# Performance work log

Measured on AMD Instinct MI355X. Metric: run time of the kernel, lower is better.

## Reference

```python
import jax, jax.numpy as jnp
import numpy as np

D_MODEL = 1024
NUM_HEADS = 16
D_K = D_MODEL // NUM_HEADS


def setup_inputs() -> dict:
    key = jax.random.key(0)
    ks = jax.random.split(key, 11)
    B, S = 2, 2048
    scale = 1.0 / np.sqrt(D_MODEL)
    inp = {
        "q": jax.random.normal(ks[0], (B, S, D_MODEL), jnp.float32),
        "k": jax.random.normal(ks[1], (B, S, D_MODEL), jnp.float32),
        "v": jax.random.normal(ks[2], (B, S, D_MODEL), jnp.float32),
        "wq": jax.random.normal(ks[3], (D_MODEL, D_MODEL), jnp.float32) * scale,
        "bq": jax.random.normal(ks[4], (D_MODEL,), jnp.float32) * 0.01,
        "wk": jax.random.normal(ks[5], (D_MODEL, D_MODEL), jnp.float32) * scale,
        "bk": jax.random.normal(ks[6], (D_MODEL,), jnp.float32) * 0.01,
        "wv": jax.random.normal(ks[7], (D_MODEL, D_MODEL), jnp.float32) * scale,
        "bv": jax.random.normal(ks[8], (D_MODEL,), jnp.float32) * 0.01,
        "wo": jax.random.normal(ks[9], (D_MODEL, D_MODEL), jnp.float32) * scale,
        "bo": jax.random.normal(ks[10], (D_MODEL,), jnp.float32) * 0.01,
    }
    return inp


def reference(q, k, v, wq, bq, wk, bk, wv, bv, wo, bo):
    B, S, _ = q.shape
    # Linear projections (torch Linear: x @ W.T + b). Weights stored [out, in].
    qh = (q @ wq.T + bq).reshape(B, S, NUM_HEADS, D_K).transpose(0, 2, 1, 3)  # [B,H,S,dk]
    kh = (k @ wk.T + bk).reshape(B, S, NUM_HEADS, D_K).transpose(0, 2, 1, 3)
    vh = (v @ wv.T + bv).reshape(B, S, NUM_HEADS, D_K).transpose(0, 2, 1, 3)
    scores = jnp.einsum("bhqd,bhkd->bhqk", qh, kh) / jnp.sqrt(jnp.asarray(D_K, qh.dtype))
    weights = jax.nn.softmax(scores, axis=-1)
    attn = jnp.einsum("bhqk,bhkd->bhqd", weights, vh)  # [B,H,S,dk]
    attn = attn.transpose(0, 2, 1, 3).reshape(B, S, D_MODEL)
    return attn @ wo.T + bo
```

## Files before the change

### kernel.cpp

```cpp
#include <hip/hip_runtime.h>

#define DM 1024
#define NH 16
#define DK 64
#define BB 2
#define SS 2048
#define MT (BB*SS)

typedef __attribute__((ext_vector_type(8))) short bf16x8;
typedef __attribute__((ext_vector_type(4))) float f32x4;

#define QSCALE 0.1803368801111191f
#define EXPC  (-14.426950408889634f)

__device__ __forceinline__ unsigned short f2bf(float f) {
    unsigned int u = __float_as_uint(f);
    u += 0x7FFF + ((u >> 16) & 1);
    return (unsigned short)(u >> 16);
}

__device__ __forceinline__ unsigned int cvt_pk_bf16(float lo, float hi) {
    unsigned int r;
    asm("v_cvt_pk_bf16_f32 %0, %1, %2" : "=v"(r) : "v"(lo), "v"(hi));
    return r;
}

__device__ __forceinline__ void gload16(const void* g, void* l) {
    __builtin_amdgcn_global_load_lds(
        (const __attribute__((address_space(1))) unsigned int*)g,
        (__attribute__((address_space(3))) unsigned int*)(unsigned int)(unsigned long long)l,
        16, 0, 0);
}

__device__ __forceinline__ int kperm(int s) {
    return (s & ~31) | (((s >> 2) & 1) << 4) | (((s >> 3) & 3) << 2) | (s & 3);
}

struct CvtArgs {
    const float* s[4];
    unsigned short* d[4];
    float scl[4];
};

__global__ __launch_bounds__(256) void cvt_f32_bf16(CvtArgs a) {
    const int arr = blockIdx.y;
    const int i = (blockIdx.x * 256 + threadIdx.x) * 8;
    const float sc = a.scl[arr];
    const float4* sp = (const float4*)(a.s[arr] + i);
    float4 x = sp[0], y = sp[1];
    union { unsigned short us[8]; uint4 u4; } r;
    r.us[0] = f2bf(x.x * sc); r.us[1] = f2bf(x.y * sc);
    r.us[2] = f2bf(x.z * sc); r.us[3] = f2bf(x.w * sc);
    r.us[4] = f2bf(y.x * sc); r.us[5] = f2bf(y.y * sc);
    r.us[6] = f2bf(y.z * sc); r.us[7] = f2bf(y.w * sc);
    *(uint4*)(a.d[arr] + i) = r.u4;
}

struct ProjArgs {
    const void* A[3];
    const void* B[3];
    const float* bias[3];
    unsigned short* out[3];
    float bscale[3];
};

__global__ __launch_bounds__(256, 3) void proj3(ProjArgs pa) {
    __shared__ __align__(16) unsigned short As[2][128 * 32];
    __shared__ __align__(16) unsigned short Bs[2][128 * 32];

    const int z = blockIdx.y;
    const int bx = blockIdx.x;
    const int xcd = bx & 7, ib = bx >> 3;
    int mb, nb;
    if (z < 2) { mb = xcd * 4 + (ib >> 3); nb = ib & 7; }
    else       { mb = ib >> 2;             nb = xcd * 4 + (ib & 3); }
    const int m0 = mb * 128, n0 = nb * 128;

    const bool a32 = (z < 2);
    const float* Af = (const float*)pa.A[z];
    const unsigned short* Ab = (const unsigned short*)pa.A[z];
    const float* Bf = (const float*)pa.B[z];
    const unsigned short* Bb = (const unsigned short*)pa.B[z];
    const float* bias = pa.bias[z];
    const float bsc = pa.bscale[z];
    unsigned short* out = pa.out[z];

    const int tid = (int)threadIdx.x;
    const int l = tid & 63;
    const int w = tid >> 6;
    const int wm = w >> 1, wn = w & 1;

    const int strow = l >> 2;
    const int sslot = (l & 3) ^ ((l >> 3) & 3);
    const int fr = l & 15, fj = l >> 4;
    const int swz = ((fj ^ ((fr >> 1) & 3)) << 4);

    const f32x4 zero = {0.f, 0.f, 0.f, 0.f};
    f32x4 acc[4][4];
    #pragma unroll
    for (int mf = 0; mf < 4; ++mf)
        #pragma unroll
        for (int nf = 0; nf < 4; ++nf) acc[mf][nf] = zero;

    #pragma unroll
    for (int t = 0; t < 2; ++t) {
        const int c = w * 2 + t;
        const int row = c * 16 + strow;
        const int col = sslot * 8;
        if (a32) {
            const float4* s = (const float4*)(Af + (size_t)(m0 + row) * DM + col);
            float4 f0 = s[0], f1 = s[1];
            union { unsigned int u[4]; bf16x8 v; } pk;
            pk.u[0] = cvt_pk_bf16(f0.x, f0.y); pk.u[1] = cvt_pk_bf16(f0.z, f0.w);
            pk.u[2] = cvt_pk_bf16(f1.x, f1.y); pk.u[3] = cvt_pk_bf16(f1.z, f1.w);
            *(bf16x8*)((char*)As[0] + c * 1024 + l * 16) = pk.v;
            gload16(Bb + (size_t)(n0 + row) * DM + col, (char*)Bs[0] + c * 1024);
        } else {
            gload16(Ab + (size_t)(m0 + row) * DM + col, (char*)As[0] + c * 1024);
            const float4* s = (const float4*)(Bf + (size_t)(n0 + row) * DM + col);
            float4 f0 = s[0], f1 = s[1];
            union { unsigned int u[4]; bf16x8 v; } pk;
            pk.u[0] = cvt_pk_bf16(f0.x, f0.y); pk.u[1] = cvt_pk_bf16(f0.z, f0.w);
            pk.u[2] = cvt_pk_bf16(f1.x, f1.y); pk.u[3] = cvt_pk_bf16(f1.z, f1.w);
            *(bf16x8*)((char*)Bs[0] + c * 1024 + l * 16) = pk.v;
        }
    }
    __syncthreads();

    for (int kt = 0; kt < DM; kt += 32) {
        const int cb = (kt >> 5) & 1;
        const bool pf = (kt + 32 < DM);
        float4 rf[2][2];
        if (pf) {
            #pragma unroll
            for (int t = 0; t < 2; ++t) {
                const int c = w * 2 + t;
                const int row = c * 16 + strow;
                const int col = kt + 32 + sslot * 8;
                if (a32) {
                    const float4* s = (const float4*)(Af + (size_t)(m0 + row) * DM + col);
                    rf[t][0] = s[0]; rf[t][1] = s[1];
                    gload16(Bb + (size_t)(n0 + row) * DM + col, (char*)Bs[cb ^ 1] + c * 1024);
                } else {
                    gload16(Ab + (size_t)(m0 + row) * DM + col, (char*)As[cb ^ 1] + c * 1024);
                    const float4* s = (const float4*)(Bf + (size_t)(n0 + row) * DM + col);
                    rf[t][0] = s[0]; rf[t][1] = s[1];
                }
            }
        }
        bf16x8 af[4], bfr[4];
        #pragma unroll
        for (int mf = 0; mf < 4; ++mf)
            af[mf] = *(const bf16x8*)((const char*)As[cb] + (wm * 64 + mf * 16 + fr) * 64 + swz);
        #pragma unroll
        for (int nf = 0; nf < 4; ++nf)
            bfr[nf] = *(const bf16x8*)((const char*)Bs[cb] + (wn * 64 + nf * 16 + fr) * 64 + swz);
        #pragma unroll
        for (int mf = 0; mf < 4; ++mf)
            #pragma unroll
            for (int nf = 0; nf < 4; ++nf)
                acc[mf][nf] = __builtin_amdgcn_mfma_f32_16x16x32_bf16(af[mf], bfr[nf], acc[mf][nf], 0, 0, 0);
        if (pf) {
            #pragma unroll
            for (int t = 0; t < 2; ++t) {
                const int c = w * 2 + t;
                union { unsigned int u[4]; bf16x8 v; } pk;
                pk.u[0] = cvt_pk_bf16(rf[t][0].x, rf[t][0].y);
                pk.u[1] = cvt_pk_bf16(rf[t][0].z, rf[t][0].w);
                pk.u[2] = cvt_pk_bf16(rf[t][1].x, rf[t][1].y);
                pk.u[3] = cvt_pk_bf16(rf[t][1].z, rf[t][1].w);
                if (a32) *(bf16x8*)((char*)As[cb ^ 1] + c * 1024 + l * 16) = pk.v;
                else     *(bf16x8*)((char*)Bs[cb ^ 1] + c * 1024 + l * 16) = pk.v;
            }
        }
        __syncthreads();
    }

    #pragma unroll
    for (int nf = 0; nf < 4; ++nf) {
        const int n = n0 + wn * 64 + nf * 16 + fr;
        const float bn = (z == 2) ? 0.f : bias[n] * bsc;
        #pragma unroll
        for (int mf = 0; mf < 4; ++mf) {
            #pragma unroll
            for (int j = 0; j < 4; ++j) {
                const int m = m0 + wm * 64 + mf * 16 + fj * 4 + j;
                if (z < 2) {
                    const float val = acc[mf][nf][j] + bn;
                    int s = m & (SS - 1);
                    if (z == 1) s = kperm(s);
                    out[((size_t)((m >> 11) * NH + (n >> 6)) * SS + s) * DK + (n & 63)] = f2bf(val);
                } else {
                    const float val = acc[mf][nf][j] + bias[m];
                    out[(size_t)((n >> 11) * NH + (m >> 6)) * (SS * DK) + (size_t)(m & 63) * SS + (n & (SS - 1))] = f2bf(val);
                }
            }
        }
    }
}

__global__ __launch_bounds__(256, 2) void gemm_out(
    const unsigned short* __restrict__ A,
    const unsigned short* __restrict__ B,
    const float* __restrict__ bias,
    float* __restrict__ out)
{
    __shared__ __align__(16) unsigned short As[2][128 * 32];
    __shared__ __align__(16) unsigned short Bs[2][64 * 32];

    const int tid = (int)threadIdx.x;
    const int l = tid & 63;
    const int w = tid >> 6;
    const int wm = w >> 1, wn = w & 1;
    const int m0 = blockIdx.x * 128, n0 = blockIdx.y * 64;

    const int strow = l >> 2;
    const int sslot = (l & 3) ^ ((l >> 3) & 3);
    const int fr = l & 15, fj = l >> 4;
    const int swz = ((fj ^ ((fr >> 1) & 3)) << 4);

    const f32x4 zero = {0.f, 0.f, 0.f, 0.f};
    f32x4 acc[4][2];
    #pragma unroll
    for (int mf = 0; mf < 4; ++mf)
        #pragma unroll
        for (int nf = 0; nf < 2; ++nf) acc[mf][nf] = zero;

    #pragma unroll
    for (int t = 0; t < 2; ++t) {
        const int c = w * 2 + t;
        gload16(A + (size_t)(m0 + c * 16 + strow) * DM + sslot * 8, (char*)As[0] + c * 1024);
    }
    gload16(B + (size_t)(n0 + w * 16 + strow) * DM + sslot * 8, (char*)Bs[0] + w * 1024);
    __syncthreads();

    for (int kt = 0; kt < DM; kt += 32) {
        const int cb = (kt >> 5) & 1;
        if (kt + 32 < DM) {
            #pragma unroll
            for (int t = 0; t < 2; ++t) {
                const int c = w * 2 + t;
                gload16(A + (size_t)(m0 + c * 16 + strow) * DM + (kt + 32) + sslot * 8, (char*)As[cb ^ 1] + c * 1024);
            }
            gload16(B + (size_t)(n0 + w * 16 + strow) * DM + (kt + 32) + sslot * 8, (char*)Bs[cb ^ 1] + w * 1024);
        }
        bf16x8 af[4], bfr[2];
        #pragma unroll
        for (int mf = 0; mf < 4; ++mf)
            af[mf] = *(const bf16x8*)((const char*)As[cb] + (wm * 64 + mf * 16 + fr) * 64 + swz);
        #pragma unroll
        for (int nf = 0; nf < 2; ++nf)
            bfr[nf] = *(const bf16x8*)((const char*)Bs[cb] + (wn * 32 + nf * 16 + fr) * 64 + swz);
        #pragma unroll
        for (int mf = 0; mf < 4; ++mf)
            #pragma unroll
            for (int nf = 0; nf < 2; ++nf)
                acc[mf][nf] = __builtin_amdgcn_mfma_f32_16x16x32_bf16(af[mf], bfr[nf], acc[mf][nf], 0, 0, 0);
        __syncthreads();
    }

    #pragma unroll
    for (int nf = 0; nf < 2; ++nf) {
        const int n = n0 + wn * 32 + nf * 16 + fr;
        const float bn = bias[n];
        #pragma unroll
        for (int mf = 0; mf < 4; ++mf)
            #pragma unroll
            for (int j = 0; j < 4; ++j) {
                const int m = m0 + wm * 64 + mf * 16 + fj * 4 + j;
                out[(size_t)m * DM + n] = acc[mf][nf][j] + bn;
            }
    }
}

__global__ __launch_bounds__(256, 2) void attn_bf16(
    const unsigned short* __restrict__ qh,
    const unsigned short* __restrict__ kh,
    const unsigned short* __restrict__ vt,
    unsigned short* __restrict__ ao)
{
    __shared__ __align__(16) unsigned short Ks[2][128 * 64];
    __shared__ __align__(16) unsigned short Vs[2][2][64 * 64];

    const int tid = (int)threadIdx.x;
    const int l = tid & 63;
    const int w = tid >> 6;
    const int bh = blockIdx.x;
    const int q0 = blockIdx.y * 128;
    const size_t pb = (size_t)bh * (SS * DK);

    const int fr = l & 15, fj = l >> 4;
    const int s8 = fr & 7;
    const int strow = l >> 3;
    const int sslot = (l & 7) ^ strow;

    bf16x8 qreg[2][2];
    #pragma unroll
    for (int qf = 0; qf < 2; ++qf)
        #pragma unroll
        for (int ks = 0; ks < 2; ++ks)
            qreg[qf][ks] = *(const bf16x8*)(qh + pb + (size_t)(q0 + w * 32 + qf * 16 + fr) * DK + ks * 32 + fj * 8);

    #pragma unroll
    for (int t = 0; t < 4; ++t) {
        const int c = w * 4 + t;
        gload16(kh + pb + (size_t)(c * 8 + strow) * DK + sslot * 8, (char*)Ks[0] + c * 1024);
    }
    #pragma unroll
    for (int s = 0; s < 2; ++s)
        #pragma unroll
        for (int tt = 0; tt < 2; ++tt) {
            const int ch = w * 2 + tt;
            gload16(vt + pb + (size_t)(ch * 8 + strow) * SS + s * 64 + sslot * 8, (char*)Vs[0][s] + ch * 1024);
        }
    asm volatile("s_waitcnt vmcnt(0)" ::: "memory");
    __syncthreads();

    const f32x4 zero = {0.f, 0.f, 0.f, 0.f};
    f32x4 ot[4][2];
    f32x4 lacc[2];
    #pragma unroll
    for (int nf = 0; nf < 4; ++nf)
        #pragma unroll
        for (int qf = 0; qf < 2; ++qf) ot[nf][qf] = zero;
    lacc[0] = zero; lacc[1] = zero;

    const int NT = SS / 128;
    for (int t = 0; t < NT; ++t) {
        const int c = t & 1;
        if (t + 1 < NT) {
            #pragma unroll
            for (int t4 = 0; t4 < 4; ++t4) {
                const int ch = w * 4 + t4;
                gload16(kh + pb + (size_t)((t + 1) * 128 + ch * 8 + strow) * DK + sslot * 8,
                        (char*)Ks[c ^ 1] + ch * 1024);
            }
        }
        f32x4 sc[8][2];
        #pragma unroll
        for (int kf = 0; kf < 8; ++kf)
            #pragma unroll
            for (int qf = 0; qf < 2; ++qf) sc[kf][qf] = zero;
        __builtin_amdgcn_s_setprio(1);
        #pragma unroll
        for (int ks = 0; ks < 2; ++ks) {
            bf16x8 kfr[8];
            #pragma unroll
            for (int kf = 0; kf < 8; ++kf)
                kfr[kf] = *(const bf16x8*)((const char*)Ks[c] + (kf * 16 + fr) * 128 + (((ks * 4 + fj) ^ s8) << 4));
            #pragma unroll
            for (int kf = 0; kf < 8; ++kf)
                #pragma unroll
                for (int qf = 0; qf < 2; ++qf)
                    sc[kf][qf] = __builtin_amdgcn_mfma_f32_16x16x32_bf16(kfr[kf], qreg[qf][ks], sc[kf][qf], 0, 0, 0);
        }
        __builtin_amdgcn_s_setprio(0);

        bf16x8 pbf[2][4];
        #pragma unroll
        for (int qf = 0; qf < 2; ++qf) {
            #pragma unroll
            for (int kss = 0; kss < 4; ++kss) {
                union { unsigned int u[4]; bf16x8 v; } pk;
                #pragma unroll
                for (int kf = 0; kf < 2; ++kf) {
                    const f32x4 s4 = sc[kss * 2 + kf][qf];
                    const float e0 = __builtin_amdgcn_exp2f(s4[0] + EXPC);
                    const float e1 = __builtin_amdgcn_exp2f(s4[1] + EXPC);
                    const float e2 = __builtin_amdgcn_exp2f(s4[2] + EXPC);
                    const float e3 = __builtin_amdgcn_exp2f(s4[3] + EXPC);
                    lacc[qf][0] += e0; lacc[qf][1] += e1;
                    lacc[qf][2] += e2; lacc[qf][3] += e3;
                    pk.u[kf * 2 + 0] = cvt_pk_bf16(e0, e1);
                    pk.u[kf * 2 + 1] = cvt_pk_bf16(e2, e3);
                }
                pbf[qf][kss] = pk.v;
            }
        }

        __builtin_amdgcn_sched_barrier(0);
        asm volatile("s_waitcnt vmcnt(0) lgkmcnt(0)" ::: "memory");
        __builtin_amdgcn_s_barrier();
        __builtin_amdgcn_sched_barrier(0);

        if (t + 1 < NT) {
            #pragma unroll
            for (int s = 0; s < 2; ++s)
                #pragma unroll
                for (int tt = 0; tt < 2; ++tt) {
                    const int ch = w * 2 + tt;
                    gload16(vt + pb + (size_t)(ch * 8 + strow) * SS + (t + 1) * 128 + s * 64 + sslot * 8,
                            (char*)Vs[c ^ 1][s] + ch * 1024);
                }
        }

        __builtin_amdgcn_s_setprio(1);
        #pragma unroll
        for (int kss = 0; kss < 4; ++kss) {
            const int sub = kss >> 1, kw = kss & 1;
            bf16x8 va[4];
            #pragma unroll
            for (int nf = 0; nf < 4; ++nf)
                va[nf] = *(const bf16x8*)((const char*)Vs[c][sub] + (nf * 16 + fr) * 128 + (((kw * 4 + fj) ^ s8) << 4));
            #pragma unroll
            for (int nf = 0; nf < 4; ++nf)
                #pragma unroll
                for (int qf = 0; qf < 2; ++qf)
                    ot[nf][qf] = __builtin_amdgcn_mfma_f32_16x16x32_bf16(va[nf], pbf[qf][kss], ot[nf][qf], 0, 0, 0);
        }
        __builtin_amdgcn_s_setprio(0);
    }

    float inv[2];
    #pragma unroll
    for (int qf = 0; qf < 2; ++qf) {
        float s = (lacc[qf][0] + lacc[qf][1]) + (lacc[qf][2] + lacc[qf][3]);
        s += __shfl_xor(s, 16);
        s += __shfl_xor(s, 32);
        inv[qf] = 1.0f / s;
    }
    const int b = bh >> 4, h = bh & 15;
    #pragma unroll
    for (int qf = 0; qf < 2; ++qf) {
        const int qg = q0 + w * 32 + qf * 16 + fr;
        unsigned short* dst = ao + (size_t)(b * SS + qg) * DM + h * DK + fj * 4;
        #pragma unroll
        for (int nf = 0; nf < 4; ++nf) {
            uint2 pw;
            pw.x = cvt_pk_bf16(ot[nf][qf][0] * inv[qf], ot[nf][qf][1] * inv[qf]);
            pw.y = cvt_pk_bf16(ot[nf][qf][2] * inv[qf], ot[nf][qf][3] * inv[qf]);
            *(uint2*)(dst + nf * 16) = pw;
        }
    }
}

extern "C" void kernel_launch(void* const* d_in, const int* in_sizes, int n_in,
                              void* d_out, int out_size, void* d_ws, size_t ws_size,
                              hipStream_t stream) {
    const float* q  = (const float*)d_in[0];
    const float* k  = (const float*)d_in[1];
    const float* v  = (const float*)d_in[2];
    const float* wq = (const float*)d_in[3];
    const float* bq = (const float*)d_in[4];
    const float* wk = (const float*)d_in[5];
    const float* bk = (const float*)d_in[6];
    const float* wv = (const float*)d_in[7];
    const float* bv = (const float*)d_in[8];
    const float* wo = (const float*)d_in[9];
    const float* bo = (const float*)d_in[10];

    const size_t NQ = (size_t)MT * DM;
    const size_t NW = (size_t)DM * DM;
    unsigned short* wsb = (unsigned short*)d_ws;
    unsigned short* wqb = wsb;
    unsigned short* wkb = wqb + NW;
    unsigned short* wvb = wkb + NW;
    unsigned short* wob = wvb + NW;
    unsigned short* qhb = wob + NW;
    unsigned short* khb = qhb + NQ;
    unsigned short* vtb = khb + NQ;
    unsigned short* aob = vtb + NQ;

    CvtArgs ca;
    ca.s[0] = wq; ca.d[0] = wqb; ca.scl[0] = QSCALE;
    ca.s[1] = wk; ca.d[1] = wkb; ca.scl[1] = 1.f;
    ca.s[2] = wv; ca.d[2] = wvb; ca.scl[2] = 1.f;
    ca.s[3] = wo; ca.d[3] = wob; ca.scl[3] = 1.f;
    cvt_f32_bf16<<<dim3(512, 4), dim3(256), 0, stream>>>(ca);

    ProjArgs pa;
    pa.A[0] = q;   pa.B[0] = wqb; pa.bias[0] = bq; pa.out[0] = qhb; pa.bscale[0] = QSCALE;
    pa.A[1] = k;   pa.B[1] = wkb; pa.bias[1] = bk; pa.out[1] = khb; pa.bscale[1] = 1.f;
    pa.A[2] = wvb; pa.B[2] = v;   pa.bias[2] = bv; pa.out[2] = vtb; pa.bscale[2] = 1.f;
    proj3<<<dim3(256, 3), dim3(256), 0, stream>>>(pa);

    attn_bf16<<<dim3(32, 16), dim3(256), 0, stream>>>(qhb, khb, vtb, aob);

    gemm_out<<<dim3(32, 16), dim3(256), 0, stream>>>(aob, wob, bo, (float*)d_out);
}
```

Before: 113.0 us.

## Prefetch fp32 operand two K-steps ahead via register ping-pong in proj3

Restructures the projection GEMM main loop so the fp32 operand's global loads are issued two K-tiles ahead into alternating register buffers. The loop is unrolled by two with a lambda body so the buffer roles stay static. The a32/non-a32 branches are unified by selecting source pointers and LDS buffers up front. This aims to hide global load latency of the fp32-to-bf16 converted operand, at the cost of extra registers that may pressure occupancy at 3 blocks per CU.

```diff
diff --git a/kernel.cpp b/kernel.cpp
--- a/kernel.cpp
+++ b/kernel.cpp
@@ -77,10 +77,13 @@
     const int m0 = mb * 128, n0 = nb * 128;
 
     const bool a32 = (z < 2);
-    const float* Af = (const float*)pa.A[z];
-    const unsigned short* Ab = (const unsigned short*)pa.A[z];
-    const float* Bf = (const float*)pa.B[z];
-    const unsigned short* Bb = (const unsigned short*)pa.B[z];
+    const float* Fsrc = (const float*)(a32 ? pa.A[z] : pa.B[z]);
+    const unsigned short* Gsrc = (const unsigned short*)(a32 ? pa.B[z] : pa.A[z]);
+    const int f0r = a32 ? m0 : n0;
+    const int g0r = a32 ? n0 : m0;
+    unsigned short* const Fb[2] = { a32 ? As[0] : Bs[0], a32 ? As[1] : Bs[1] };
+    unsigned short* const Gb[2] = { a32 ? Bs[0] : As[0], a32 ? Bs[1] : As[1] };
+
     const float* bias = pa.bias[z];
     const float bsc = pa.bscale[z];
     unsigned short* out = pa.out[z];
@@ -102,50 +105,44 @@
         #pragma unroll
         for (int nf = 0; nf < 4; ++nf) acc[mf][nf] = zero;
 
+    float4 r0[2][2], r1[2][2];
+
     #pragma unroll
     for (int t = 0; t < 2; ++t) {
         const int c = w * 2 + t;
         const int row = c * 16 + strow;
         const int col = sslot * 8;
-        if (a32) {
-            const float4* s = (const float4*)(Af + (size_t)(m0 + row) * DM + col);
-            float4 f0 = s[0], f1 = s[1];
-            union { unsigned int u[4]; bf16x8 v; } pk;
-            pk.u[0] = cvt_pk_bf16(f0.x, f0.y); pk.u[1] = cvt_pk_bf16(f0.z, f0.w);
-            pk.u[2] = cvt_pk_bf16(f1.x, f1.y); pk.u[3] = cvt_pk_bf16(f1.z, f1.w);
-            *(bf16x8*)((char*)As[0] + c * 1024 + l * 16) = pk.v;
-            gload16(Bb + (size_t)(n0 + row) * DM + col, (char*)Bs[0] + c * 1024);
-        } else {
-            gload16(Ab + (size_t)(m0 + row) * DM + col, (char*)As[0] + c * 1024);
-            const float4* s = (const float4*)(Bf + (size_t)(n0 + row) * DM + col);
-            float4 f0 = s[0], f1 = s[1];
-            union { unsigned int u[4]; bf16x8 v; } pk;
-            pk.u[0] = cvt_pk_bf16(f0.x, f0.y); pk.u[1] = cvt_pk_bf16(f0.z, f0.w);
-            pk.u[2] = cvt_pk_bf16(f1.x, f1.y); pk.u[3] = cvt_pk_bf16(f1.z, f1.w);
-            *(bf16x8*)((char*)Bs[0] + c * 1024 + l * 16) = pk.v;
-        }
+        const float4* s = (const float4*)(Fsrc + (size_t)(f0r + row) * DM + col);
+        float4 f0v = s[0], f1v = s[1];
+        union { unsigned int u[4]; bf16x8 v; } pk;
+        pk.u[0] = cvt_pk_bf16(f0v.x, f0v.y); pk.u[1] = cvt_pk_bf16(f0v.z, f0v.w);
+        pk.u[2] = cvt_pk_bf16(f1v.x, f1v.y); pk.u[3] = cvt_pk_bf16(f1v.z, f1v.w);
+        *(bf16x8*)((char*)Fb[0] + c * 1024 + l * 16) = pk.v;
+        gload16(Gsrc + (size_t)(g0r + row) * DM + col, (char*)Gb[0] + c * 1024);
+    }
+    #pragma unroll
+    for (int t = 0; t < 2; ++t) {
+        const int row = (w * 2 + t) * 16 + strow;
+        const float4* s = (const float4*)(Fsrc + (size_t)(f0r + row) * DM + 32 + sslot * 8);
+        r0[t][0] = s[0]; r0[t][1] = s[1];
     }
     __syncthreads();
 
-    for (int kt = 0; kt < DM; kt += 32) {
-        const int cb = (kt >> 5) & 1;
-        const bool pf = (kt + 32 < DM);
-        float4 rf[2][2];
-        if (pf) {
+    auto body = [&](int k, int cb, float4 (&rin)[2][2], float4 (&rout)[2][2]) {
+        if (k + 64 < DM) {
+            #pragma unroll
+            for (int t = 0; t < 2; ++t) {
+                const int row = (w * 2 + t) * 16 + strow;
+                const float4* s = (const float4*)(Fsrc + (size_t)(f0r + row) * DM + (k + 64) + sslot * 8);
+                rout[t][0] = s[0]; rout[t][1] = s[1];
+            }
+        }
+        if (k + 32 < DM) {
             #pragma unroll
             for (int t = 0; t < 2; ++t) {
                 const int c = w * 2 + t;
                 const int row = c * 16 + strow;
-                const int col = kt + 32 + sslot * 8;
-                if (a32) {
-                    const float4* s = (const float4*)(Af + (size_t)(m0 + row) * DM + col);
-                    rf[t][0] = s[0]; rf[t][1] = s[1];
-                    gload16(Bb + (size_t)(n0 + row) * DM + col, (char*)Bs[cb ^ 1] + c * 1024);
-                } else {
-                    gload16(Ab + (size_t)(m0 + row) * DM + col, (char*)As[cb ^ 1] + c * 1024);
-                    const float4* s = (const float4*)(Bf + (size_t)(n0 + row) * DM + col);
-                    rf[t][0] = s[0]; rf[t][1] = s[1];
-                }
+                gload16(Gsrc + (size_t)(g0r + row) * DM + (k + 32) + sslot * 8, (char*)Gb[cb ^ 1] + c * 1024);
             }
         }
         bf16x8 af[4], bfr[4];
@@ -160,20 +157,24 @@
             #pragma unroll
             for (int nf = 0; nf < 4; ++nf)
                 acc[mf][nf] = __builtin_amdgcn_mfma_f32_16x16x32_bf16(af[mf], bfr[nf], acc[mf][nf], 0, 0, 0);
-        if (pf) {
+        if (k + 32 < DM) {
             #pragma unroll
             for (int t = 0; t < 2; ++t) {
                 const int c = w * 2 + t;
                 union { unsigned int u[4]; bf16x8 v; } pk;
-                pk.u[0] = cvt_pk_bf16(rf[t][0].x, rf[t][0].y);
-                pk.u[1] = cvt_pk_bf16(rf[t][0].z, rf[t][0].w);
-                pk.u[2] = cvt_pk_bf16(rf[t][1].x, rf[t][1].y);
-                pk.u[3] = cvt_pk_bf16(rf[t][1].z, rf[t][1].w);
-                if (a32) *(bf16x8*)((char*)As[cb ^ 1] + c * 1024 + l * 16) = pk.v;
-                else     *(bf16x8*)((char*)Bs[cb ^ 1] + c * 1024 + l * 16) = pk.v;
+                pk.u[0] = cvt_pk_bf16(rin[t][0].x, rin[t][0].y);
+                pk.u[1] = cvt_pk_bf16(rin[t][0].z, rin[t][0].w);
+                pk.u[2] = cvt_pk_bf16(rin[t][1].x, rin[t][1].y);
+                pk.u[3] = cvt_pk_bf16(rin[t][1].z, rin[t][1].w);
+                *(bf16x8*)((char*)Fb[cb ^ 1] + c * 1024 + l * 16) = pk.v;
             }
         }
         __syncthreads();
+    };
+
+    for (int kt = 0; kt < DM; kt += 64) {
+        body(kt, 0, r0, r1);
+        body(kt + 32, 1, r1, r0);
     }
 
     #pragma unroll
```

Result: no change. 112.7 us (-0.3%).
